# Kernel tuning notes

Hardware: AMD Instinct MI355X
Metric: run time of the kernel (lower is better)

Reference implementation:

```python
import jax, jax.numpy as jnp
import numpy as np

N = 4096      # num nodes
F = 64        # input feature dim
H = 8         # head_num
D = 8         # att_embedding_size


def setup_inputs() -> dict:
    key = jax.random.key(0)
    k1, k2, k3, k4, k5, k6 = jax.random.split(key, 6)
    X = jax.random.normal(k1, (N, F), dtype=jnp.float32)
    # sparse-ish binary adjacency with self loops (avg degree ~ 41)
    A = (jax.random.uniform(k2, (N, N)) < 0.01).astype(jnp.float32)
    A = jnp.maximum(A, jnp.eye(N, dtype=jnp.float32))
    # glorot-uniform-ish parameter init
    lim_w = np.sqrt(6.0 / (F + H * D)).astype(np.float32)
    W = jax.random.uniform(k3, (F, H * D), minval=-lim_w, maxval=lim_w, dtype=jnp.float32)
    lim_a = np.sqrt(6.0 / (1 + H * D)).astype(np.float32)
    att_self = jax.random.uniform(k4, (H, D), minval=-lim_a, maxval=lim_a, dtype=jnp.float32)
    att_neigh = jax.random.uniform(k5, (H, D), minval=-lim_a, maxval=lim_a, dtype=jnp.float32)
    bias = jnp.zeros((H, D), dtype=jnp.float32)
    return {"X": X, "A": A, "W": W, "att_self": att_self, "att_neigh": att_neigh, "bias": bias}


def reference(X, A, W, att_self, att_neigh, bias):
    # features: [N, H, D]
    feats = (X @ W).reshape(-1, H, D)
    # additive attention logits per node/head: [N, H]
    a_self = jnp.einsum('nhd,hd->nh', feats, att_self)
    a_neigh = jnp.einsum('nhd,hd->nh', feats, att_neigh)
    # scores[h, i, j] = a_self[i, h] + a_neigh[j, h]  -> [H, N, N]
    scores = a_self.T[:, :, None] + a_neigh.T[:, None, :]
    scores = jax.nn.leaky_relu(scores, negative_slope=0.2)
    # adjacency mask: -1e10 where no edge
    scores = scores + (-1e10 * (1.0 - A))[None, :, :]
    attn = jax.nn.softmax(scores, axis=-1)           # [H, N, N]
    # aggregate: [H, N, N] x [N, H, D] -> [N, H, D]
    out = jnp.einsum('hij,jhd->ihd', attn, feats)
    out = out + bias[None, :, :]                     # use_bias
    out = out.reshape(-1, H * D)                     # reduction='concat'
    return jax.nn.relu(out)                          # activation=relu
```

## Files before the change

kernel.cpp:

```cpp
#include <hip/hip_runtime.h>
#include <hip/hip_bf16.h>

#define NNODES 4096
#define NF 64
#define NH 8
#define ND 8
#define HD 64
#define EMAX 128
#define SCAP 32
#define NFEAT (NNODES / 4)

__device__ __forceinline__ float ldv(const void* p, int i, bool f32) {
    return f32 ? ((const float*)p)[i]
               : __bfloat162float(((const __hip_bfloat16*)p)[i]);
}

__device__ __forceinline__ void ld8(const void* base, int idx, bool f32, float* o) {
    if (f32) {
        const float4* p = (const float4*)((const float*)base + idx);
        float4 a = p[0], b = p[1];
        o[0]=a.x; o[1]=a.y; o[2]=a.z; o[3]=a.w;
        o[4]=b.x; o[5]=b.y; o[6]=b.z; o[7]=b.w;
    } else {
        uint4 u = *(const uint4*)((const unsigned short*)base + idx);
        unsigned int ws[4] = {u.x, u.y, u.z, u.w};
        #pragma unroll
        for (int q = 0; q < 4; ++q) {
            o[2*q]   = __uint_as_float(ws[q] << 16);
            o[2*q+1] = __uint_as_float(ws[q] & 0xffff0000u);
        }
    }
}

__device__ __forceinline__ bool a_is_f32(const void* A) {
    return *(const unsigned int*)A == 0x3F800000u;
}

__device__ __forceinline__ unsigned int bits_bf16(uint4 p0, uint4 p1) {
    unsigned int bits = 0;
    unsigned int w0[4] = {p0.x, p0.y, p0.z, p0.w};
    unsigned int w1[4] = {p1.x, p1.y, p1.z, p1.w};
    #pragma unroll
    for (int q = 0; q < 4; ++q) {
        if (w0[q] & 0x0000ffffu) bits |= 1u << (2 * q);
        if (w0[q] & 0xffff0000u) bits |= 1u << (2 * q + 1);
        if (w1[q] & 0x0000ffffu) bits |= 1u << (8 + 2 * q);
        if (w1[q] & 0xffff0000u) bits |= 1u << (8 + 2 * q + 1);
    }
    return bits;
}
__device__ __forceinline__ unsigned int bits_f32(const uint4* c) {
    unsigned int bits = 0;
    #pragma unroll
    for (int q = 0; q < 4; ++q) {
        if (c[q].x) bits |= 1u << (4 * q + 0);
        if (c[q].y) bits |= 1u << (4 * q + 1);
        if (c[q].z) bits |= 1u << (4 * q + 2);
        if (c[q].w) bits |= 1u << (4 * q + 3);
    }
    return bits;
}

__device__ __forceinline__ void scatter_row(
    unsigned int bits, int i, int wave, int lane, int col0,
    unsigned short* __restrict__ elist, unsigned int* __restrict__ ecnt4)
{
    int cnt = __popc(bits);
    int incl = cnt;
    #pragma unroll
    for (int off = 1; off < 64; off <<= 1) {
        int nn = __shfl_up(incl, off, 64);
        if (lane >= off) incl += nn;
    }
    int pos = incl - cnt;
    unsigned short* seg = elist + i * EMAX + wave * SCAP;
    unsigned int mb = bits;
    while (mb) {
        int b = __ffs(mb) - 1; mb &= mb - 1;
        if (pos < SCAP) seg[pos] = (unsigned short)(col0 + b);
        ++pos;
    }
    if (lane == 63) {
        int tot = (incl < SCAP) ? incl : SCAP;
        ((unsigned char*)ecnt4)[i * 4 + wave] = (unsigned char)tot;
    }
}

__global__ __launch_bounds__(256) void gat_fused(
    const void* __restrict__ X,
    const void* __restrict__ W,
    const void* __restrict__ att_self,
    const void* __restrict__ att_neigh,
    const void* __restrict__ A,
    float* __restrict__ feats,
    float* __restrict__ a_self,
    float* __restrict__ a_neigh,
    unsigned short* __restrict__ elist,
    unsigned int* __restrict__ ecnt4)
{
    const bool f32 = a_is_f32(A);
    const int t = threadIdx.x;
    __shared__ float Wl[NF][HD];
    __shared__ float Xl[4][NF];

    if (blockIdx.x < NFEAT) {
        {
            float wv[16];
            ld8(W, t * 16,     f32, wv);
            ld8(W, t * 16 + 8, f32, wv + 8);
            const int row = t >> 2, col0 = (t & 3) * 16;
            #pragma unroll
            for (int k = 0; k < 16; ++k) Wl[row][col0 + k] = wv[k];
        }
        if (t < 32) {
            const int row = t >> 3, col = (t & 7) * 8;
            float xv[8];
            ld8(X, (blockIdx.x * 4 + row) * NF + col, f32, xv);
            #pragma unroll
            for (int k = 0; k < 8; ++k) Xl[row][col + k] = xv[k];
        }
        __syncthreads();

        const int r = t >> 6, c = t & 63;
        float acc = 0.f;
        #pragma unroll
        for (int k = 0; k < NF; ++k)
            acc = fmaf(Xl[r][k], Wl[k][c], acc);

        const int n = blockIdx.x * 4 + r;
        feats[n * HD + c] = acc;

        const int d = c & 7, h = c >> 3;
        float vs = acc * ldv(att_self, c, f32);
        float vn = acc * ldv(att_neigh, c, f32);
        #pragma unroll
        for (int off = 1; off < 8; off <<= 1) {
            vs += __shfl_xor(vs, off, 64);
            vn += __shfl_xor(vn, off, 64);
        }
        if (d == 0) {
            a_self[n * NH + h]  = vs;
            a_neigh[n * NH + h] = vn;
        }
    } else {
        const int i0 = (blockIdx.x - NFEAT) * 4;
        const int wave = t >> 6, lane = t & 63;
        const int col0 = t * 16;

        if (f32) {
            const float* Af = (const float*)A;
            uint4 c[4], n[4];
            {
                const uint4* rp = (const uint4*)(Af + (size_t)i0 * NNODES + col0);
                #pragma unroll
                for (int q = 0; q < 4; ++q) c[q] = rp[q];
            }
            #pragma unroll
            for (int r = 0; r < 4; ++r) {
                if (r < 3) {
                    const uint4* rp = (const uint4*)(Af + (size_t)(i0 + r + 1) * NNODES + col0);
                    #pragma unroll
                    for (int q = 0; q < 4; ++q) n[q] = rp[q];
                }
                scatter_row(bits_f32(c), i0 + r, wave, lane, col0, elist, ecnt4);
                #pragma unroll
                for (int q = 0; q < 4; ++q) c[q] = n[q];
            }
        } else {
            const unsigned short* Ab = (const unsigned short*)A;
            uint4 c0, c1, n0, n1;
            {
                const uint4* rp = (const uint4*)(Ab + (size_t)i0 * NNODES + col0);
                c0 = rp[0]; c1 = rp[1];
            }
            #pragma unroll
            for (int r = 0; r < 4; ++r) {
                if (r < 3) {
                    const uint4* rp = (const uint4*)(Ab + (size_t)(i0 + r + 1) * NNODES + col0);
                    n0 = rp[0]; n1 = rp[1];
                }
                scatter_row(bits_bf16(c0, c1), i0 + r, wave, lane, col0, elist, ecnt4);
                c0 = n0; c1 = n1;
            }
        }
    }
}

__global__ __launch_bounds__(256) void gat_gather(
    const unsigned short* __restrict__ elist,
    const unsigned int* __restrict__ ecnt4,
    const float* __restrict__ feats,
    const float* __restrict__ a_self_g,
    const float* __restrict__ a_neigh,
    const void* __restrict__ bias,
    const void* __restrict__ A,
    float* __restrict__ out)
{
    const bool f32 = a_is_f32(A);
    const int i = blockIdx.x;
    const int t = threadIdx.x;
    const int wave = t >> 6, lane = t & 63;
    const int c = lane, h = c >> 3, d = c & 7;

    __shared__ float red[4][HD];
    __shared__ float dsh[4][NH];

    const unsigned short* seg = elist + i * EMAX + wave * SCAP;
    uint4 id0 = ((const uint4*)seg)[0];
    uint4 id1 = ((const uint4*)seg)[1];
    const unsigned int cnts = ecnt4[i];
    const float ash = a_self_g[i * NH + h];
    const int cw = (cnts >> (wave * 8)) & 0xff;

    float acc = 0.f, den = 0.f;

    {
        unsigned int q[8] = {id0.x, id0.y, id0.z, id0.w, id1.x, id1.y, id1.z, id1.w};
        int j[16];
        #pragma unroll
        for (int k = 0; k < 16; ++k) {
            int id = (q[k >> 1] >> ((k & 1) * 16)) & 0xffff;
            j[k] = (k < cw) ? id : i;
        }
        float an[16], fv[16];
        #pragma unroll
        for (int k = 0; k < 16; ++k) an[k] = a_neigh[j[k] * NH + h];
        #pragma unroll
        for (int k = 0; k < 16; ++k) fv[k] = feats[j[k] * HD + c];
        #pragma unroll
        for (int k = 0; k < 16; ++k) {
            float aa = (k < cw) ? an[k] : -1e30f;
            float s = ash + aa;
            s = (s >= 0.f) ? s : 0.2f * s;
            float wt = __expf(s);
            acc = fmaf(wt, fv[k], acc);
            den += wt;
        }
    }
    if (cw > 16) {
        uint4 id2 = ((const uint4*)seg)[2];
        uint4 id3 = ((const uint4*)seg)[3];
        unsigned int q[8] = {id2.x, id2.y, id2.z, id2.w, id3.x, id3.y, id3.z, id3.w};
        int j[16];
        #pragma unroll
        for (int k = 0; k < 16; ++k) {
            int id = (q[k >> 1] >> ((k & 1) * 16)) & 0xffff;
            j[k] = (16 + k < cw) ? id : i;
        }
        float an[16], fv[16];
        #pragma unroll
        for (int k = 0; k < 16; ++k) an[k] = a_neigh[j[k] * NH + h];
        #pragma unroll
        for (int k = 0; k < 16; ++k) fv[k] = feats[j[k] * HD + c];
        #pragma unroll
        for (int k = 0; k < 16; ++k) {
            float aa = (16 + k < cw) ? an[k] : -1e30f;
            float s = ash + aa;
            s = (s >= 0.f) ? s : 0.2f * s;
            float wt = __expf(s);
            acc = fmaf(wt, fv[k], acc);
            den += wt;
        }
    }

    red[wave][c] = acc;
    if (d == 0) dsh[wave][h] = den;
    __syncthreads();

    if (t < HD) {
        float tot = red[0][t] + red[1][t] + red[2][t] + red[3][t];
        int hh = t >> 3;
        float dd = dsh[0][hh] + dsh[1][hh] + dsh[2][hh] + dsh[3][hh];
        float v = tot / dd + ldv(bias, t, f32);
        out[(size_t)i * HD + t] = fmaxf(v, 0.f);
    }
}

extern "C" void kernel_launch(void* const* d_in, const int* in_sizes, int n_in,
                              void* d_out, int out_size, void* d_ws, size_t ws_size,
                              hipStream_t stream) {
    const void* X         = d_in[0];
    const void* A         = d_in[1];
    const void* W         = d_in[2];
    const void* att_self  = d_in[3];
    const void* att_neigh = d_in[4];
    const void* bias      = d_in[5];
    float* out = (float*)d_out;

    float* feats   = (float*)d_ws;
    float* a_self  = feats  + NNODES * HD;
    float* a_neigh = a_self + NNODES * NH;
    unsigned int* ecnt4 = (unsigned int*)(a_neigh + NNODES * NH);
    unsigned short* elist = (unsigned short*)(ecnt4 + NNODES);

    gat_fused<<<NFEAT + NNODES / 4, 256, 0, stream>>>(
        X, W, att_self, att_neigh, A, feats, a_self, a_neigh, elist, ecnt4);
    gat_gather<<<NNODES, 256, 0, stream>>>(
        elist, ecnt4, feats, a_self, a_neigh, bias, A, out);
}
```

Measured before the change: 28.51 us.

## Merge feature-projection and adjacency-scan blocks, overlap A prefetch with matmul

Each block now handles both the X@W projection and the adjacency scatter for the same 4 rows, so the grid is halved. The first two A rows are loaded before the projection FMA loop runs, which hides load latency behind compute, and the prefetch depth goes from one row ahead to two. In exchange, every block now loads W into shared memory (it did not before) and holds more registers for the deeper prefetch, which may reduce occupancy.

```diff
diff --git a/kernel.cpp b/kernel.cpp
--- a/kernel.cpp
+++ b/kernel.cpp
@@ -8,7 +8,6 @@
 #define HD 64
 #define EMAX 128
 #define SCAP 32
-#define NFEAT (NNODES / 4)
 
 __device__ __forceinline__ float ldv(const void* p, int i, bool f32) {
     return f32 ? ((const float*)p)[i]
@@ -100,88 +99,115 @@
 {
     const bool f32 = a_is_f32(A);
     const int t = threadIdx.x;
+    const int wid = t >> 6, lane = t & 63;
+    const int i0 = blockIdx.x * 4;
+    const int col0 = t * 16;
+
     __shared__ float Wl[NF][HD];
     __shared__ float Xl[4][NF];
 
-    if (blockIdx.x < NFEAT) {
+    {
+        float wv[16];
+        ld8(W, t * 16,     f32, wv);
+        ld8(W, t * 16 + 8, f32, wv + 8);
+        const int row = t >> 2, c0 = (t & 3) * 16;
+        #pragma unroll
+        for (int k = 0; k < 16; ++k) Wl[row][c0 + k] = wv[k];
+    }
+    if (t < 32) {
+        const int row = t >> 3, col = (t & 7) * 8;
+        float xv[8];
+        ld8(X, (i0 + row) * NF + col, f32, xv);
+        #pragma unroll
+        for (int k = 0; k < 8; ++k) Xl[row][col + k] = xv[k];
+    }
+    __syncthreads();
+
+    if (f32) {
+        const float* Af = (const float*)A;
+        uint4 c[4], n[4];
         {
-            float wv[16];
-            ld8(W, t * 16,     f32, wv);
-            ld8(W, t * 16 + 8, f32, wv + 8);
-            const int row = t >> 2, col0 = (t & 3) * 16;
-            #pragma unroll
-            for (int k = 0; k < 16; ++k) Wl[row][col0 + k] = wv[k];
-        }
-        if (t < 32) {
-            const int row = t >> 3, col = (t & 7) * 8;
-            float xv[8];
-            ld8(X, (blockIdx.x * 4 + row) * NF + col, f32, xv);
-            #pragma unroll
-            for (int k = 0; k < 8; ++k) Xl[row][col + k] = xv[k];
-        }
-        __syncthreads();
-
-        const int r = t >> 6, c = t & 63;
-        float acc = 0.f;
-        #pragma unroll
-        for (int k = 0; k < NF; ++k)
-            acc = fmaf(Xl[r][k], Wl[k][c], acc);
-
-        const int n = blockIdx.x * 4 + r;
-        feats[n * HD + c] = acc;
-
-        const int d = c & 7, h = c >> 3;
-        float vs = acc * ldv(att_self, c, f32);
-        float vn = acc * ldv(att_neigh, c, f32);
-        #pragma unroll
-        for (int off = 1; off < 8; off <<= 1) {
-            vs += __shfl_xor(vs, off, 64);
-            vn += __shfl_xor(vn, off, 64);
-        }
-        if (d == 0) {
-            a_self[n * NH + h]  = vs;
-            a_neigh[n * NH + h] = vn;
+            const uint4* rp = (const uint4*)(Af + (size_t)i0 * NNODES + col0);
+            #pragma unroll
+            for (int q = 0; q < 4; ++q) c[q] = rp[q];
+            const uint4* rp1 = (const uint4*)(Af + (size_t)(i0 + 1) * NNODES + col0);
+            #pragma unroll
+            for (int q = 0; q < 4; ++q) n[q] = rp1[q];
+        }
+
+        {
+            float acc = 0.f;
+            #pragma unroll
+            for (int k = 0; k < NF; ++k)
+                acc = fmaf(Xl[wid][k], Wl[k][lane], acc);
+            const int nrow = i0 + wid;
+            feats[nrow * HD + lane] = acc;
+            const int d = lane & 7, h = lane >> 3;
+            float vs = acc * ldv(att_self, lane, f32);
+            float vn = acc * ldv(att_neigh, lane, f32);
+            #pragma unroll
+            for (int off = 1; off < 8; off <<= 1) {
+                vs += __shfl_xor(vs, off, 64);
+                vn += __shfl_xor(vn, off, 64);
+            }
+            if (d == 0) {
+                a_self[nrow * NH + h]  = vs;
+                a_neigh[nrow * NH + h] = vn;
+            }
+        }
+
+        #pragma unroll
+        for (int r = 0; r < 4; ++r) {
+            uint4 t4[4];
+            if (r < 2) {
+                const uint4* rp = (const uint4*)(Af + (size_t)(i0 + r + 2) * NNODES + col0);
+                #pragma unroll
+                for (int q = 0; q < 4; ++q) t4[q] = rp[q];
+            }
+            scatter_row(bits_f32(c), i0 + r, wid, lane, col0, elist, ecnt4);
+            #pragma unroll
+            for (int q = 0; q < 4; ++q) { c[q] = n[q]; n[q] = t4[q]; }
         }
     } else {
-        const int i0 = (blockIdx.x - NFEAT) * 4;
-        const int wave = t >> 6, lane = t & 63;
-        const int col0 = t * 16;
-
-        if (f32) {
-            const float* Af = (const float*)A;
-            uint4 c[4], n[4];
-            {
-                const uint4* rp = (const uint4*)(Af + (size_t)i0 * NNODES + col0);
-                #pragma unroll
-                for (int q = 0; q < 4; ++q) c[q] = rp[q];
-            }
-            #pragma unroll
-            for (int r = 0; r < 4; ++r) {
-                if (r < 3) {
-                    const uint4* rp = (const uint4*)(Af + (size_t)(i0 + r + 1) * NNODES + col0);
-                    #pragma unroll
-                    for (int q = 0; q < 4; ++q) n[q] = rp[q];
-                }
-                scatter_row(bits_f32(c), i0 + r, wave, lane, col0, elist, ecnt4);
-                #pragma unroll
-                for (int q = 0; q < 4; ++q) c[q] = n[q];
-            }
-        } else {
-            const unsigned short* Ab = (const unsigned short*)A;
-            uint4 c0, c1, n0, n1;
-            {
-                const uint4* rp = (const uint4*)(Ab + (size_t)i0 * NNODES + col0);
-                c0 = rp[0]; c1 = rp[1];
-            }
-            #pragma unroll
-            for (int r = 0; r < 4; ++r) {
-                if (r < 3) {
-                    const uint4* rp = (const uint4*)(Ab + (size_t)(i0 + r + 1) * NNODES + col0);
-                    n0 = rp[0]; n1 = rp[1];
-                }
-                scatter_row(bits_bf16(c0, c1), i0 + r, wave, lane, col0, elist, ecnt4);
-                c0 = n0; c1 = n1;
-            }
+        const unsigned short* Ab = (const unsigned short*)A;
+        uint4 c0, c1, n0, n1;
+        {
+            const uint4* rp = (const uint4*)(Ab + (size_t)i0 * NNODES + col0);
+            c0 = rp[0]; c1 = rp[1];
+            const uint4* rp1 = (const uint4*)(Ab + (size_t)(i0 + 1) * NNODES + col0);
+            n0 = rp1[0]; n1 = rp1[1];
+        }
+
+        {
+            float acc = 0.f;
+            #pragma unroll
+            for (int k = 0; k < NF; ++k)
+                acc = fmaf(Xl[wid][k], Wl[k][lane], acc);
+            const int nrow = i0 + wid;
+            feats[nrow * HD + lane] = acc;
+            const int d = lane & 7, h = lane >> 3;
+            float vs = acc * ldv(att_self, lane, f32);
+            float vn = acc * ldv(att_neigh, lane, f32);
+            #pragma unroll
+            for (int off = 1; off < 8; off <<= 1) {
+                vs += __shfl_xor(vs, off, 64);
+                vn += __shfl_xor(vn, off, 64);
+            }
+            if (d == 0) {
+                a_self[nrow * NH + h]  = vs;
+                a_neigh[nrow * NH + h] = vn;
+            }
+        }
+
+        #pragma unroll
+        for (int r = 0; r < 4; ++r) {
+            uint4 t0, t1;
+            if (r < 2) {
+                const uint4* rp = (const uint4*)(Ab + (size_t)(i0 + r + 2) * NNODES + col0);
+                t0 = rp[0]; t1 = rp[1];
+            }
+            scatter_row(bits_bf16(c0, c1), i0 + r, wid, lane, col0, elist, ecnt4);
+            c0 = n0; c1 = n1; n0 = t0; n1 = t1;
         }
     }
 }
@@ -293,7 +319,7 @@
     unsigned int* ecnt4 = (unsigned int*)(a_neigh + NNODES * NH);
     unsigned short* elist = (unsigned short*)(ecnt4 + NNODES);
 
-    gat_fused<<<NFEAT + NNODES / 4, 256, 0, stream>>>(
+    gat_fused<<<NNODES / 4, 256, 0, stream>>>(
         X, W, att_self, att_neigh, A, feats, a_self, a_neigh, elist, ecnt4);
     gat_gather<<<NNODES, 256, 0, stream>>>(
         elist, ecnt4, feats, a_self, a_neigh, bias, A, out);
```

Measured after the change: 28.68 us. No clear change (+0.6%).
